# Kernel optimization log

Hardware: AMD Instinct MI355X
Metric: run time of the kernel (lower is better)

Reference implementation:

```python
import jax, jax.numpy as jnp
import numpy as np

SEQ_LEN = 262144
N = 128  # number of event types


def setup_inputs() -> dict:
    key = jax.random.key(0)
    k_in, k_q, k_k = jax.random.split(key, 3)
    scale = 1.0 / np.sqrt(N)  # matches nn.Linear default init scale
    Input = jax.random.normal(k_in, (SEQ_LEN, N), dtype=jnp.float32)
    W_Q = jax.random.uniform(k_q, (N, N), dtype=jnp.float32, minval=-scale, maxval=scale)
    W_K = jax.random.uniform(k_k, (N, N), dtype=jnp.float32, minval=-scale, maxval=scale)
    return {"Input": Input, "W_Q": W_Q, "W_K": W_K}


def reference(Input, W_Q, W_K):
    # Original loops over one-hot type rows e_t:
    #   query_t = e_t @ W_Q.T = W_Q[:, t]
    #   keys    = Input @ W_K.T                         (S, N)
    #   aw[:,t] = softplus(keys @ query_t)
    #   Output[s,t] = aw[s,t] * sum_j Input[s,j]
    # Fused/batched form:
    keys = Input @ W_K.T                                 # (S, N)
    aw = jax.nn.softplus(keys @ W_Q)                     # (S, N), col t uses W_Q[:, t]
    row_sum = jnp.sum(Input, axis=1, keepdims=True)      # (S, 1)
    Output = aw * row_sum                                # (S, N)
    loss = jnp.mean((Output[:-1] - Input[1:]) ** 2)
    l1 = jnp.sum(jnp.abs(jax.nn.sigmoid(W_K.T @ W_Q)))
    return (loss, l1)
```

## Files before the change

kernel.cpp:

```cpp
#include <hip/hip_runtime.h>
#include <math.h>

#define S_LEN 262144
#define N 128
#define BR 64
#define TPB 256
#define NT (S_LEN / BR)
#define GRID 1024
#define TILES_PER_BLOCK (NT / GRID)

typedef __attribute__((ext_vector_type(8))) short bf16x8;
typedef __attribute__((ext_vector_type(4))) float f32x4;

__device__ __forceinline__ unsigned short f2bf(float x) {
    unsigned b = __float_as_uint(x);
    b = (b + 0x7FFF + ((b >> 16) & 1)) >> 16;
    return (unsigned short)b;
}
__device__ __forceinline__ float bf2f(unsigned short u) {
    return __uint_as_float((unsigned)u << 16);
}
__device__ __forceinline__ unsigned pack2bf(float x, float y) {
    return __builtin_amdgcn_perm(__float_as_uint(y) + 0x8000u,
                                 __float_as_uint(x) + 0x8000u, 0x07060302u);
}
__device__ __forceinline__ float wave_reduce(float v) {
    #pragma unroll
    for (int off = 32; off > 0; off >>= 1) v += __shfl_down(v, off, 64);
    return v;
}
__device__ __forceinline__ void gld16(const float* g, float* l) {
    __builtin_amdgcn_global_load_lds(
        (const __attribute__((address_space(1))) unsigned int*)g,
        (__attribute__((address_space(3))) unsigned int*)l, 16, 0, 0);
}

__global__ void mk_kernel(const float* __restrict__ WQ, const float* __restrict__ WK,
                          unsigned short* __restrict__ fragB, float* __restrict__ out) {
    const int i = blockIdx.x;
    const int j = threadIdx.x;
    float acc = 0.f;
    #pragma unroll 8
    for (int r = 0; r < N; ++r) acc = fmaf(WK[r * N + i], WQ[r * N + j], acc);

    const int kk = i >> 5, q = (i >> 3) & 3, jj = i & 7;
    const int ct = j >> 4, n15 = j & 15;
    fragB[((kk * 8 + ct) * 64 + (q * 16 + n15)) * 8 + jj] = f2bf(acc);

    float sg = fabsf(1.0f / (1.0f + __expf(-acc)));
    float ws = wave_reduce(sg);
    __shared__ float red[2];
    if ((j & 63) == 0) red[j >> 6] = ws;
    __syncthreads();
    if (j == 0) atomicAdd(&out[1], red[0] + red[1]);
}

__global__ __launch_bounds__(TPB, 3) void main_kernel(
    const float* __restrict__ In, const unsigned short* __restrict__ fragB,
    float* __restrict__ out, float inv_denom) {
    __shared__ float F[BR * N];
    __shared__ unsigned short sA[65][136];
    __shared__ float sRed[TPB / 64];

    const int tid = threadIdx.x;
    const int w = tid >> 6, lane = tid & 63;
    const int q = lane >> 4, n15 = lane & 15;

    bf16x8 bF[2][4];
    #pragma unroll
    for (int c = 0; c < 2; ++c)
        #pragma unroll
        for (int kk = 0; kk < 4; ++kk)
            bF[c][kk] = *(const bf16x8*)&fragB[((kk * 8 + (w * 2 + c)) * 64 + lane) * 8];

    bf16x8 bOne;
    #pragma unroll
    for (int e = 0; e < 8; ++e) bOne[e] = (short)0x3F80;

    float lsum = 0.f;
    float4 x;
    int tile = blockIdx.x;

    {
        const float* gb = In + (size_t)tile * BR * N;
        #pragma unroll
        for (int j = 0; j < 8; ++j) {
            const int ci = w * 8 + j;
            gld16(gb + ci * 256 + lane * 4, &F[ci * 256]);
        }
        long rX = (long)tile * BR + BR; if (rX > S_LEN - 1) rX = S_LEN - 1;
        if (tid < 32) x = *(const float4*)&In[rX * N + (tid << 2)];
    }

    for (int it = 0; it < TILES_PER_BLOCK; ++it) {
        asm volatile("s_waitcnt vmcnt(0)" ::: "memory");
        __syncthreads();

        #pragma unroll
        for (int t = 0; t < 8; ++t) {
            const int qq = tid + t * TPB;
            const int r = qq >> 5, c4 = (qq & 31) << 2;
            const float4 v = *(const float4*)&F[r * N + c4];
            *(uint2*)&sA[r][c4] = make_uint2(pack2bf(v.x, v.y), pack2bf(v.z, v.w));
        }
        if (tid < 32)
            *(uint2*)&sA[64][tid << 2] = make_uint2(pack2bf(x.x, x.y), pack2bf(x.z, x.w));
        __syncthreads();

        if (it + 1 < TILES_PER_BLOCK) {
            const int nt2 = tile + GRID;
            const float* gb = In + (size_t)nt2 * BR * N;
            #pragma unroll
            for (int j = 0; j < 8; ++j) {
                const int ci = w * 8 + j;
                gld16(gb + ci * 256 + lane * 4, &F[ci * 256]);
            }
            long rX = (long)nt2 * BR + BR; if (rX > S_LEN - 1) rX = S_LEN - 1;
            if (tid < 32) x = *(const float4*)&In[rX * N + (tid << 2)];
        }

        f32x4 acc[4][2], accRS[4];
        #pragma unroll
        for (int rt = 0; rt < 4; ++rt) {
            accRS[rt] = (f32x4){0.f, 0.f, 0.f, 0.f};
            #pragma unroll
            for (int c = 0; c < 2; ++c) acc[rt][c] = (f32x4){0.f, 0.f, 0.f, 0.f};
        }
        #pragma unroll
        for (int rt = 0; rt < 4; ++rt) {
            #pragma unroll
            for (int kk = 0; kk < 4; ++kk) {
                bf16x8 a = *(const bf16x8*)&sA[rt * 16 + n15][kk * 32 + q * 8];
                accRS[rt] = __builtin_amdgcn_mfma_f32_16x16x32_bf16(a, bOne, accRS[rt], 0, 0, 0);
                #pragma unroll
                for (int c = 0; c < 2; ++c)
                    acc[rt][c] = __builtin_amdgcn_mfma_f32_16x16x32_bf16(a, bF[c][kk], acc[rt][c], 0, 0, 0);
            }
        }

        const long r0 = (long)tile * BR;
        #pragma unroll
        for (int rt = 0; rt < 4; ++rt) {
            #pragma unroll
            for (int reg = 0; reg < 4; ++reg) {
                const int row = rt * 16 + q * 4 + reg;
                const float rs = accRS[rt][reg];
                const long s = r0 + row;
                const bool has = (s < S_LEN - 1);
                #pragma unroll
                for (int c = 0; c < 2; ++c) {
                    const float z = acc[rt][c][reg];
                    const float sp = fmaxf(z, 0.f) + __logf(1.0f + __expf(-fabsf(z)));
                    const float o = sp * rs;
                    if (has) {
                        const int col = w * 32 + c * 16 + n15;
                        const float d = o - bf2f(sA[row + 1][col]);
                        lsum = fmaf(d, d, lsum);
                    }
                }
            }
        }
        tile += GRID;
    }

    const float wsum = wave_reduce(lsum);
    if ((tid & 63) == 0) sRed[w] = wsum;
    __syncthreads();
    if (tid == 0) {
        float t = 0.f;
        #pragma unroll
        for (int w2 = 0; w2 < TPB / 64; ++w2) t += sRed[w2];
        atomicAdd(&out[0], t * inv_denom);
    }
}

extern "C" void kernel_launch(void* const* d_in, const int* in_sizes, int n_in,
                              void* d_out, int out_size, void* d_ws, size_t ws_size,
                              hipStream_t stream) {
    const float* In = (const float*)d_in[0];
    const float* WQ = (const float*)d_in[1];
    const float* WK = (const float*)d_in[2];
    float* out = (float*)d_out;
    unsigned short* fragB = (unsigned short*)d_ws;

    hipMemsetAsync(d_out, 0, 2 * sizeof(float), stream);
    mk_kernel<<<128, 128, 0, stream>>>(WQ, WK, fragB, out);
    const float inv = (float)(1.0 / ((double)(S_LEN - 1) * (double)N));
    main_kernel<<<GRID, TPB, 0, stream>>>(In, fragB, out, inv);
}
```

Measured before the change: 215.1 us.

## Restructure tile loop to prefetch next tile earlier and trim barriers

Each wave now reads its own slice of the staged fp32 tile into registers, and the next tile's global-to-LDS load is issued right after those reads instead of after the bf16 conversion barrier. The cross-wave barrier is also moved so only one or two raw barriers guard the sA buffer per tile. The grid drops from 1024 to 768 blocks with a while loop over a non-uniform tile count, and the sA row padding changes from 136 to 132. The aim is to overlap the global load with conversion and compute and to cut synchronisation. The costs are extra register pressure, possible LDS bank conflicts from the new padding, and load imbalance from the uneven tile count per block.

Measured after the change: 213.8 us. About the same (-0.6%).

```diff
diff --git a/kernel.cpp b/kernel.cpp
--- a/kernel.cpp
+++ b/kernel.cpp
@@ -6,8 +6,7 @@
 #define BR 64
 #define TPB 256
 #define NT (S_LEN / BR)
-#define GRID 1024
-#define TILES_PER_BLOCK (NT / GRID)
+#define GRID 768
 
 typedef __attribute__((ext_vector_type(8))) short bf16x8;
 typedef __attribute__((ext_vector_type(4))) float f32x4;
@@ -34,6 +33,9 @@
         (const __attribute__((address_space(1))) unsigned int*)g,
         (__attribute__((address_space(3))) unsigned int*)l, 16, 0, 0);
 }
+__device__ __forceinline__ void wait_vm0()   { asm volatile("s_waitcnt vmcnt(0)" ::: "memory"); }
+__device__ __forceinline__ void wait_lgkm0() { asm volatile("s_waitcnt lgkmcnt(0)" ::: "memory"); }
+__device__ __forceinline__ void barrier_raw(){ asm volatile("s_waitcnt lgkmcnt(0)\ns_barrier" ::: "memory"); }
 
 __global__ void mk_kernel(const float* __restrict__ WQ, const float* __restrict__ WK,
                           unsigned short* __restrict__ fragB, float* __restrict__ out) {
@@ -59,7 +61,7 @@
     const float* __restrict__ In, const unsigned short* __restrict__ fragB,
     float* __restrict__ out, float inv_denom) {
     __shared__ float F[BR * N];
-    __shared__ unsigned short sA[65][136];
+    __shared__ unsigned short sA[65][132];
     __shared__ float sRed[TPB / 64];
 
     const int tid = threadIdx.x;
@@ -79,9 +81,8 @@
 
     float lsum = 0.f;
     float4 x;
-    int tile = blockIdx.x;
 
-    {
+    auto issue = [&](int tile) {
         const float* gb = In + (size_t)tile * BR * N;
         #pragma unroll
         for (int j = 0; j < 8; ++j) {
@@ -90,34 +91,36 @@
         }
         long rX = (long)tile * BR + BR; if (rX > S_LEN - 1) rX = S_LEN - 1;
         if (tid < 32) x = *(const float4*)&In[rX * N + (tid << 2)];
-    }
+    };
 
-    for (int it = 0; it < TILES_PER_BLOCK; ++it) {
-        asm volatile("s_waitcnt vmcnt(0)" ::: "memory");
-        __syncthreads();
+    int tile = blockIdx.x;
+    bool first = true;
+    issue(tile);
 
+    while (tile < NT) {
+        const int next = tile + GRID;
+
+        wait_vm0();
+        const float4 xc = x;
+        float4 r[8];
         #pragma unroll
         for (int t = 0; t < 8; ++t) {
-            const int qq = tid + t * TPB;
-            const int r = qq >> 5, c4 = (qq & 31) << 2;
-            const float4 v = *(const float4*)&F[r * N + c4];
-            *(uint2*)&sA[r][c4] = make_uint2(pack2bf(v.x, v.y), pack2bf(v.z, v.w));
+            const int row = w * 16 + t * 2 + (lane >> 5);
+            r[t] = *(const float4*)&F[row * N + ((lane & 31) << 2)];
+        }
+        wait_lgkm0();
+        if (next < NT) issue(next);
+
+        if (!first) barrier_raw();
+        #pragma unroll
+        for (int t = 0; t < 8; ++t) {
+            const int row = w * 16 + t * 2 + (lane >> 5);
+            *(uint2*)&sA[row][(lane & 31) << 2] =
+                make_uint2(pack2bf(r[t].x, r[t].y), pack2bf(r[t].z, r[t].w));
         }
         if (tid < 32)
-            *(uint2*)&sA[64][tid << 2] = make_uint2(pack2bf(x.x, x.y), pack2bf(x.z, x.w));
-        __syncthreads();
-
-        if (it + 1 < TILES_PER_BLOCK) {
-            const int nt2 = tile + GRID;
-            const float* gb = In + (size_t)nt2 * BR * N;
-            #pragma unroll
-            for (int j = 0; j < 8; ++j) {
-                const int ci = w * 8 + j;
-                gld16(gb + ci * 256 + lane * 4, &F[ci * 256]);
-            }
-            long rX = (long)nt2 * BR + BR; if (rX > S_LEN - 1) rX = S_LEN - 1;
-            if (tid < 32) x = *(const float4*)&In[rX * N + (tid << 2)];
-        }
+            *(uint2*)&sA[64][tid << 2] = make_uint2(pack2bf(xc.x, xc.y), pack2bf(xc.z, xc.w));
+        barrier_raw();
 
         f32x4 acc[4][2], accRS[4];
         #pragma unroll
@@ -160,7 +163,8 @@
                 }
             }
         }
-        tile += GRID;
+        tile = next;
+        first = false;
     }
 
     const float wsum = wave_reduce(lsum);
```
